# Optimization experiments

Hardware: AMD Instinct MI355X
Metric: run time of the kernel (lower is better)

Reference implementation:

```python
import jax, jax.numpy as jnp
import numpy as np
from jax.scipy.special import logsumexp

N, C = 8192, 4096
LOSS_WEIGHT = 1.0


def setup_inputs() -> dict:
    key = jax.random.key(0)
    k1, k2 = jax.random.split(key)
    cls_score = jax.random.normal(k1, (N, C), dtype=jnp.float32)
    label = jax.random.randint(k2, (N, C), 0, 2, dtype=jnp.int64)
    return {"cls_score": cls_score, "label": label}


def reference(cls_score, label):
    # pos/neg masks exactly as in the torch module
    pos = label >= 1
    neg = label == 0
    ninf = -jnp.inf
    # Torch builds an [N, C*C] tensor of (neg_k - pos_j) padded with a 0 column
    # and takes logsumexp over it. Algebraically:
    #   loss_i = logaddexp(0, logsumexp_k(pred[neg]) + logsumexp_j(-pred[pos]))
    lse_neg = logsumexp(jnp.where(neg, cls_score, ninf), axis=1)      # [N]
    lse_mpos = logsumexp(jnp.where(pos, -cls_score, ninf), axis=1)    # [N]
    loss = jnp.logaddexp(jnp.float32(0.0), lse_neg + lse_mpos)        # [N]
    # reduction='mean', loss_weight applied in forward
    return LOSS_WEIGHT * jnp.mean(loss)
```

## Files before the change

### kernel.cpp

```cpp
#include <hip/hip_runtime.h>
#include <hip/hip_bf16.h>
#include <float.h>

#define NROWS 8192
#define NCOLS 4096


__device__ __forceinline__ void accum_group(const float4* f, const int4* l,
                                            float& s_n, float& s_p) {
#pragma unroll
    for (int j = 0; j < 4; ++j) {
        float x[4] = {f[j].x, f[j].y, f[j].z, f[j].w};
        int   m[4] = {l[j].x, l[j].y, l[j].z, l[j].w};
#pragma unroll
        for (int k = 0; k < 4; ++k) {
            bool neg = (m[k] == 0);
            float e = __expf(neg ? x[k] : -x[k]);
            s_n += neg ? e : 0.0f;
            s_p += neg ? 0.0f : e;
        }
    }
}

__global__ __launch_bounds__(256) void row_loss_kernel(
        const float* __restrict__ score,
        const int* __restrict__ label,
        float* __restrict__ row_loss) {
    const int wave = threadIdx.x >> 6;
    const int lane = threadIdx.x & 63;
    const int row  = blockIdx.x * 4 + wave;

    const float4* __restrict__ srow = reinterpret_cast<const float4*>(score + (size_t)row * NCOLS);
    const int4*   __restrict__ lrow = reinterpret_cast<const int4*>(label + (size_t)row * NCOLS);

    float4 fa[4], fb[4];
    int4   la[4], lb[4];

#pragma unroll
    for (int j = 0; j < 4; ++j) {
        fa[j] = srow[lane + j * 64];
        la[j] = lrow[lane + j * 64];
    }

    float s_n = 0.0f, s_p = 0.0f;

#pragma unroll
    for (int j = 0; j < 4; ++j) { fb[j] = srow[256 + lane + j * 64]; lb[j] = lrow[256 + lane + j * 64]; }
    accum_group(fa, la, s_n, s_p);
#pragma unroll
    for (int j = 0; j < 4; ++j) { fa[j] = srow[512 + lane + j * 64]; la[j] = lrow[512 + lane + j * 64]; }
    accum_group(fb, lb, s_n, s_p);
#pragma unroll
    for (int j = 0; j < 4; ++j) { fb[j] = srow[768 + lane + j * 64]; lb[j] = lrow[768 + lane + j * 64]; }
    accum_group(fa, la, s_n, s_p);
    accum_group(fb, lb, s_n, s_p);

#pragma unroll
    for (int off = 32; off > 0; off >>= 1) {
        s_n += __shfl_down(s_n, off, 64);
        s_p += __shfl_down(s_p, off, 64);
    }

    if (lane == 0) {
        float loss;
        if (s_n <= 0.0f || s_p <= 0.0f) {
            loss = 0.0f;
        } else {
            float z = logf(s_n) + logf(s_p);
            loss = fmaxf(z, 0.0f) + log1pf(__expf(-fabsf(z)));
        }
        row_loss[row] = loss;
    }
}

__global__ __launch_bounds__(256) void mean_kernel(
        const float* __restrict__ row_loss,
        float* __restrict__ out) {
    const int t = threadIdx.x;
    const float4* rl = reinterpret_cast<const float4*>(row_loss);
    float s = 0.0f;
#pragma unroll
    for (int j = 0; j < NROWS / 4 / 256; ++j) {
        float4 v = rl[t + j * 256];
        s += (v.x + v.y) + (v.z + v.w);
    }
#pragma unroll
    for (int off = 32; off > 0; off >>= 1) s += __shfl_down(s, off, 64);
    __shared__ float ls[4];
    if ((t & 63) == 0) ls[t >> 6] = s;
    __syncthreads();
    if (t == 0) {
        float total = ls[0] + ls[1] + ls[2] + ls[3];
        out[0] = total * (1.0f / (float)NROWS);
    }
}

extern "C" void kernel_launch(void* const* d_in, const int* in_sizes, int n_in,
                              void* d_out, int out_size, void* d_ws, size_t ws_size,
                              hipStream_t stream) {
    const float* score = (const float*)d_in[0];
    const int*   label = (const int*)d_in[1];
    float* row_loss = (float*)d_ws;
    float* out = (float*)d_out;

    row_loss_kernel<<<NROWS / 4, 256, 0, stream>>>(score, label, row_loss);
    mean_kernel<<<1, 256, 0, stream>>>(row_loss, out);
}
```

Before: 276.8 us.

## Stream row chunks into LDS through a multi-slot async global_load_lds ring

Replaces the register double-buffered global loads with asynchronous global-to-LDS loads (global_load_lds, 16 bytes per lane). Each wave keeps a private 5-slot ring in shared memory and keeps up to four chunks of scores and labels in flight. It waits on vmcnt with explicit s_waitcnt and sched_barriers before reading each chunk back from LDS. The aim is to keep more memory traffic outstanding and lower register pressure. In exchange it uses about 40 KB of LDS per block, which can limit occupancy, and adds an extra LDS read for every element.

```diff
diff --git a/kernel.cpp b/kernel.cpp
--- a/kernel.cpp
+++ b/kernel.cpp
@@ -1,31 +1,23 @@
 #include <hip/hip_runtime.h>
 #include <hip/hip_bf16.h>
-#include <float.h>
 
 #define NROWS 8192
 #define NCOLS 4096
+#define NCHUNK 16
+#define NSLOT 5
 
 
-__device__ __forceinline__ void accum_group(const float4* f, const int4* l,
-                                            float& s_n, float& s_p) {
-#pragma unroll
-    for (int j = 0; j < 4; ++j) {
-        float x[4] = {f[j].x, f[j].y, f[j].z, f[j].w};
-        int   m[4] = {l[j].x, l[j].y, l[j].z, l[j].w};
-#pragma unroll
-        for (int k = 0; k < 4; ++k) {
-            bool neg = (m[k] == 0);
-            float e = __expf(neg ? x[k] : -x[k]);
-            s_n += neg ? e : 0.0f;
-            s_p += neg ? 0.0f : e;
-        }
-    }
-}
+typedef __attribute__((address_space(1))) const unsigned int g_u32;
+typedef __attribute__((address_space(3))) unsigned int       l_u32;
+
+#define WAITVM(n) __builtin_amdgcn_s_waitcnt(0x0F70 | (n))
 
 __global__ __launch_bounds__(256) void row_loss_kernel(
         const float* __restrict__ score,
         const int* __restrict__ label,
         float* __restrict__ row_loss) {
+    __shared__ float4 s_sc[4][NSLOT][64];
+    __shared__ int4   s_lb[4][NSLOT][64];
     const int wave = threadIdx.x >> 6;
     const int lane = threadIdx.x & 63;
     const int row  = blockIdx.x * 4 + wave;
@@ -33,27 +25,40 @@
     const float4* __restrict__ srow = reinterpret_cast<const float4*>(score + (size_t)row * NCOLS);
     const int4*   __restrict__ lrow = reinterpret_cast<const int4*>(label + (size_t)row * NCOLS);
 
-    float4 fa[4], fb[4];
-    int4   la[4], lb[4];
+#define DMA(c, s)                                                                           \
+    __builtin_amdgcn_global_load_lds((g_u32*)(srow + (c) * 64 + lane),                      \
+                                     (l_u32*)(&s_sc[wave][(s)][0]), 16, 0, 0);              \
+    __builtin_amdgcn_global_load_lds((g_u32*)(lrow + (c) * 64 + lane),                      \
+                                     (l_u32*)(&s_lb[wave][(s)][0]), 16, 0, 0);
 
-#pragma unroll
-    for (int j = 0; j < 4; ++j) {
-        fa[j] = srow[lane + j * 64];
-        la[j] = lrow[lane + j * 64];
-    }
+    DMA(0, 0) DMA(1, 1) DMA(2, 2) DMA(3, 3)
+    __builtin_amdgcn_sched_barrier(0);
 
     float s_n = 0.0f, s_p = 0.0f;
 
-#pragma unroll
-    for (int j = 0; j < 4; ++j) { fb[j] = srow[256 + lane + j * 64]; lb[j] = lrow[256 + lane + j * 64]; }
-    accum_group(fa, la, s_n, s_p);
-#pragma unroll
-    for (int j = 0; j < 4; ++j) { fa[j] = srow[512 + lane + j * 64]; la[j] = lrow[512 + lane + j * 64]; }
-    accum_group(fb, lb, s_n, s_p);
-#pragma unroll
-    for (int j = 0; j < 4; ++j) { fb[j] = srow[768 + lane + j * 64]; lb[j] = lrow[768 + lane + j * 64]; }
-    accum_group(fa, la, s_n, s_p);
-    accum_group(fb, lb, s_n, s_p);
+#define STEP(c)                                                                             \
+    {                                                                                       \
+        constexpr int pairs_out = (NCHUNK - (c)) < 4 ? (NCHUNK - (c)) : 4;                  \
+        WAITVM(2 * pairs_out - 2);             \
+        __builtin_amdgcn_sched_barrier(0);                                                  \
+        if ((c) + 4 < NCHUNK) { DMA((c) + 4, ((c) + 4) % NSLOT) }                           \
+        __builtin_amdgcn_sched_barrier(0);                                                  \
+        float4 f = s_sc[wave][(c) % NSLOT][lane];                                           \
+        int4   m = s_lb[wave][(c) % NSLOT][lane];                                           \
+        float x[4] = {f.x, f.y, f.z, f.w};                                                  \
+        int   l[4] = {m.x, m.y, m.z, m.w};                                                  \
+        _Pragma("unroll") for (int k = 0; k < 4; ++k) {                                     \
+            bool neg = (l[k] == 0);                                                         \
+            float e = __expf(neg ? x[k] : -x[k]);                                           \
+            s_n += neg ? e : 0.0f;                                                          \
+            s_p += neg ? 0.0f : e;                                                          \
+        }                                                                                   \
+    }
+
+    STEP(0)  STEP(1)  STEP(2)  STEP(3)
+    STEP(4)  STEP(5)  STEP(6)  STEP(7)
+    STEP(8)  STEP(9)  STEP(10) STEP(11)
+    STEP(12) STEP(13) STEP(14) STEP(15)
 
 #pragma unroll
     for (int off = 32; off > 0; off >>= 1) {
```

Result: no change. 275.4 us (-0.5%).

## Split rows into quarter-row chunks with persistent waves and three-stage reduction

Applied to the files above, without the earlier changes.

Replaces the one-wave-per-row kernel with a persistent grid of 1024 blocks, where each wave walks over quarter-row chunks of 1024 elements. It prefetches the next chunk while computing the current one and writes per-chunk (neg, pos) partial sums. A second kernel combines four partials per row and computes the row loss and block sums, and a third kernel takes the mean. The goal is fewer short-lived waves and better load/compute overlap on a bandwidth-bound stream. The cost is an extra kernel launch and a global round trip for the partials.

```diff
diff --git a/kernel.cpp b/kernel.cpp
--- a/kernel.cpp
+++ b/kernel.cpp
@@ -1,98 +1,99 @@
 #include <hip/hip_runtime.h>
 #include <hip/hip_bf16.h>
-#include <float.h>
 
 #define NROWS 8192
 #define NCOLS 4096
+#define NBLK 1024
+#define WAVES_TOTAL (NBLK * 4)
+#define NSC (NROWS * 4)
+#define ITERS (NSC / WAVES_TOTAL)
 
 
-__device__ __forceinline__ void accum_group(const float4* f, const int4* l,
-                                            float& s_n, float& s_p) {
+__global__ __launch_bounds__(256) void partial_kernel(
+        const float* __restrict__ score,
+        const int* __restrict__ label,
+        float2* __restrict__ part) {
+    const int wgid = blockIdx.x * 4 + (threadIdx.x >> 6);
+    const int lane = threadIdx.x & 63;
+    const float4* __restrict__ s4 = reinterpret_cast<const float4*>(score);
+    const int4*   __restrict__ l4 = reinterpret_cast<const int4*>(label);
+
+    int g = wgid;
+    float4 fa[4]; int4 la[4];
 #pragma unroll
     for (int j = 0; j < 4; ++j) {
-        float x[4] = {f[j].x, f[j].y, f[j].z, f[j].w};
-        int   m[4] = {l[j].x, l[j].y, l[j].z, l[j].w};
+        fa[j] = s4[(size_t)g * 256 + j * 64 + lane];
+        la[j] = l4[(size_t)g * 256 + j * 64 + lane];
+    }
+
 #pragma unroll
-        for (int k = 0; k < 4; ++k) {
-            bool neg = (m[k] == 0);
-            float e = __expf(neg ? x[k] : -x[k]);
-            s_n += neg ? e : 0.0f;
-            s_p += neg ? 0.0f : e;
+    for (int it = 0; it < ITERS; ++it) {
+        const int gn = g + WAVES_TOTAL;
+        float4 fb[4]; int4 lb[4];
+        if (it + 1 < ITERS) {
+#pragma unroll
+            for (int j = 0; j < 4; ++j) {
+                fb[j] = s4[(size_t)gn * 256 + j * 64 + lane];
+                lb[j] = l4[(size_t)gn * 256 + j * 64 + lane];
+            }
         }
+        float sn = 0.0f, sp = 0.0f;
+#pragma unroll
+        for (int j = 0; j < 4; ++j) {
+            float x[4] = {fa[j].x, fa[j].y, fa[j].z, fa[j].w};
+            int   m[4] = {la[j].x, la[j].y, la[j].z, la[j].w};
+#pragma unroll
+            for (int k = 0; k < 4; ++k) {
+                bool neg = (m[k] == 0);
+                float e = __expf(neg ? x[k] : -x[k]);
+                sn += neg ? e : 0.0f;
+                sp += neg ? 0.0f : e;
+            }
+        }
+#pragma unroll
+        for (int off = 32; off > 0; off >>= 1) {
+            sn += __shfl_down(sn, off, 64);
+            sp += __shfl_down(sp, off, 64);
+        }
+        if (lane == 0) part[g] = make_float2(sn, sp);
+        if (it + 1 < ITERS) {
+#pragma unroll
+            for (int j = 0; j < 4; ++j) { fa[j] = fb[j]; la[j] = lb[j]; }
+        }
+        g = gn;
     }
 }
 
-__global__ __launch_bounds__(256) void row_loss_kernel(
-        const float* __restrict__ score,
-        const int* __restrict__ label,
-        float* __restrict__ row_loss) {
-    const int wave = threadIdx.x >> 6;
-    const int lane = threadIdx.x & 63;
-    const int row  = blockIdx.x * 4 + wave;
-
-    const float4* __restrict__ srow = reinterpret_cast<const float4*>(score + (size_t)row * NCOLS);
-    const int4*   __restrict__ lrow = reinterpret_cast<const int4*>(label + (size_t)row * NCOLS);
-
-    float4 fa[4], fb[4];
-    int4   la[4], lb[4];
-
+__global__ __launch_bounds__(128) void row_reduce_kernel(
+        const float2* __restrict__ part,
+        float* __restrict__ blocksum) {
+    const int r = blockIdx.x * 128 + threadIdx.x;
+    const float4* __restrict__ p4 = reinterpret_cast<const float4*>(part);
+    float4 a = p4[2 * r], b = p4[2 * r + 1];
+    float sn = (a.x + a.z) + (b.x + b.z);
+    float sp = (a.y + a.w) + (b.y + b.w);
+    float loss;
+    if (sn <= 0.0f || sp <= 0.0f) {
+        loss = 0.0f;
+    } else {
+        float z = logf(sn) + logf(sp);
+        loss = fmaxf(z, 0.0f) + log1pf(__expf(-fabsf(z)));
+    }
 #pragma unroll
-    for (int j = 0; j < 4; ++j) {
-        fa[j] = srow[lane + j * 64];
-        la[j] = lrow[lane + j * 64];
-    }
-
-    float s_n = 0.0f, s_p = 0.0f;
-
-#pragma unroll
-    for (int j = 0; j < 4; ++j) { fb[j] = srow[256 + lane + j * 64]; lb[j] = lrow[256 + lane + j * 64]; }
-    accum_group(fa, la, s_n, s_p);
-#pragma unroll
-    for (int j = 0; j < 4; ++j) { fa[j] = srow[512 + lane + j * 64]; la[j] = lrow[512 + lane + j * 64]; }
-    accum_group(fb, lb, s_n, s_p);
-#pragma unroll
-    for (int j = 0; j < 4; ++j) { fb[j] = srow[768 + lane + j * 64]; lb[j] = lrow[768 + lane + j * 64]; }
-    accum_group(fa, la, s_n, s_p);
-    accum_group(fb, lb, s_n, s_p);
-
-#pragma unroll
-    for (int off = 32; off > 0; off >>= 1) {
-        s_n += __shfl_down(s_n, off, 64);
-        s_p += __shfl_down(s_p, off, 64);
-    }
-
-    if (lane == 0) {
-        float loss;
-        if (s_n <= 0.0f || s_p <= 0.0f) {
-            loss = 0.0f;
-        } else {
-            float z = logf(s_n) + logf(s_p);
-            loss = fmaxf(z, 0.0f) + log1pf(__expf(-fabsf(z)));
-        }
-        row_loss[row] = loss;
-    }
+    for (int off = 32; off > 0; off >>= 1) loss += __shfl_down(loss, off, 64);
+    __shared__ float ls[2];
+    if ((threadIdx.x & 63) == 0) ls[threadIdx.x >> 6] = loss;
+    __syncthreads();
+    if (threadIdx.x == 0) blocksum[blockIdx.x] = ls[0] + ls[1];
 }
 
-__global__ __launch_bounds__(256) void mean_kernel(
-        const float* __restrict__ row_loss,
+__global__ __launch_bounds__(64) void final_kernel(
+        const float* __restrict__ blocksum,
         float* __restrict__ out) {
-    const int t = threadIdx.x;
-    const float4* rl = reinterpret_cast<const float4*>(row_loss);
-    float s = 0.0f;
-#pragma unroll
-    for (int j = 0; j < NROWS / 4 / 256; ++j) {
-        float4 v = rl[t + j * 256];
-        s += (v.x + v.y) + (v.z + v.w);
-    }
+    float s = blocksum[threadIdx.x];
 #pragma unroll
     for (int off = 32; off > 0; off >>= 1) s += __shfl_down(s, off, 64);
-    __shared__ float ls[4];
-    if ((t & 63) == 0) ls[t >> 6] = s;
-    __syncthreads();
-    if (t == 0) {
-        float total = ls[0] + ls[1] + ls[2] + ls[3];
-        out[0] = total * (1.0f / (float)NROWS);
-    }
+    if (threadIdx.x == 0) out[0] = s * (1.0f / (float)NROWS);
 }
 
 extern "C" void kernel_launch(void* const* d_in, const int* in_sizes, int n_in,
@@ -100,9 +101,11 @@
                               hipStream_t stream) {
     const float* score = (const float*)d_in[0];
     const int*   label = (const int*)d_in[1];
-    float* row_loss = (float*)d_ws;
-    float* out = (float*)d_out;
+    float2* part     = (float2*)d_ws;
+    float*  blocksum = (float*)((char*)d_ws + NSC * 8);
+    float*  out      = (float*)d_out;
 
-    row_loss_kernel<<<NROWS / 4, 256, 0, stream>>>(score, label, row_loss);
-    mean_kernel<<<1, 256, 0, stream>>>(row_loss, out);
+    partial_kernel<<<NBLK, 256, 0, stream>>>(score, label, part);
+    row_reduce_kernel<<<NROWS / 128, 128, 0, stream>>>(part, blocksum);
+    final_kernel<<<1, 64, 0, stream>>>(blocksum, out);
 }
```

Result: no change. 274.4 us (-0.9%).
